# Kernel optimization log

Measured on AMD Instinct MI355X. Metric: run time of the kernel, lower is better.

Reference implementation:

```python
import jax, jax.numpy as jnp
import numpy as np

B_SZ = 4; SEQ = 2048; D_INPUT = 40; D_MODEL = 128; N_LAYERS = 4
D_STATE = 16; EXPAND = 2; D_INNER = D_MODEL * EXPAND
N_HEADS = 4; D_HEAD = D_MODEL // N_HEADS; MAX_LANDMARKS = 100
EPS_RMS = 1.1920929e-07  # torch nn.RMSNorm default eps = finfo(float32).eps
EPS_LN = 1e-5
A_FLOOR = 1e-4


def _rms(x, w):
    return x * jax.lax.rsqrt(jnp.mean(x * x, -1, keepdims=True) + EPS_RMS) * w


def _ln(x, w, b):
    m = jnp.mean(x, -1, keepdims=True)
    v = jnp.mean((x - m) ** 2, -1, keepdims=True)
    return (x - m) * jax.lax.rsqrt(v + EPS_LN) * w + b


def _mamba3_block(xin, Wi, Wx, Wdt, bdt, Alog, Bb, Cb, Bnw, Cnw, rf, Dv, Wo):
    # xin: (B,L,d_model)
    xz = xin @ Wi                       # (B,L,2*d_inner)
    xp, z = jnp.split(xz, 2, axis=-1)
    xp = jax.nn.silu(xp)
    sp = xp @ Wx                        # (B,L,2*d_state+2)
    B_raw = sp[..., :D_STATE]
    C_raw = sp[..., D_STATE:2 * D_STATE]
    dt_in = sp[..., -2:-1]
    lam_in = sp[..., -1:]
    Bm = _rms(B_raw + Bb, Bnw)
    Cm = _rms(C_raw + Cb, Cnw)
    dt = jax.nn.softplus(dt_in @ Wdt + bdt)   # (B,L,d_inner)
    lam = jax.nn.sigmoid(lam_in)              # (B,L,1)
    # data-dependent RoPE on B and C
    freqs = jax.nn.softplus(rf)                                  # (d_state//2,)
    ang = jnp.cumsum(jnp.mean(dt, -1, keepdims=True), axis=1) * freqs  # (B,L,ds/2)
    ca, sa = jnp.cos(ang), jnp.sin(ang)

    def rot(M):
        e, o = M[..., ::2], M[..., 1::2]
        return jnp.stack([e * ca - o * sa, e * sa + o * ca], -1).reshape(M.shape)

    Bm, Cm = rot(Bm), rot(Cm)
    A = jnp.minimum(-jnp.exp(Alog), -A_FLOOR)   # (d_inner,d_state)
    dte = dt[..., None]                          # (B,L,d_inner,1)
    dA = jnp.exp(A * dte)                        # (B,L,d_inner,d_state)
    Bx = Bm[:, :, None, :] * xp[..., None]       # (B,L,d_inner,d_state)
    Bx_prev = jnp.concatenate([jnp.zeros_like(Bx[:, :1]), Bx[:, :-1]], axis=1)
    lame = lam[..., None]                        # (B,L,1,1)
    u = (1.0 - lame) * dte * dA * Bx_prev + lame * dte * Bx
    u = u.at[:, 0].set(dte[:, 0] * Bx[:, 0])     # t==0 case: h = dt*B*x (no lambda)

    def step(h, inp):
        dA_t, u_t, C_t = inp
        h = dA_t * h + u_t
        return h, jnp.sum(h * C_t[:, None, :], -1)

    h0 = jnp.zeros((xin.shape[0], D_INNER, D_STATE), xin.dtype)
    _, ys = jax.lax.scan(step, h0, (jnp.swapaxes(dA, 0, 1), jnp.swapaxes(u, 0, 1), jnp.swapaxes(Cm, 0, 1)))
    y = jnp.swapaxes(ys, 0, 1)                   # (B,L,d_inner)
    y = y + xp * Dv
    y = y * jax.nn.silu(z)
    return y @ Wo


def _landmark_attn(mo, skip, hw, WQ, bQ, WK, bK, WV, bV, WO, bO):
    Bsz, L, Dm = skip.shape
    k = min(MAX_LANDMARKS, L)
    _, idx = jax.lax.top_k(hw, k)
    idx = jnp.sort(idx, axis=1)                            # (B,k)
    kv = jnp.take_along_axis(skip, idx[..., None], axis=1)  # (B,k,Dm)
    q = mo[:, -1:, :]                                       # (B,1,Dm)
    Q = (q @ WQ + bQ).reshape(Bsz, 1, N_HEADS, D_HEAD).transpose(0, 2, 1, 3)
    K = (kv @ WK + bK).reshape(Bsz, k, N_HEADS, D_HEAD).transpose(0, 2, 1, 3)
    V = (kv @ WV + bV).reshape(Bsz, k, N_HEADS, D_HEAD).transpose(0, 2, 1, 3)
    scores = jnp.einsum('bhqd,bhkd->bhqk', Q, K) * (D_HEAD ** -0.5)
    probs = jax.nn.softmax(scores, axis=-1)
    out = jnp.einsum('bhqk,bhkd->bhqd', probs, V).transpose(0, 2, 1, 3).reshape(Bsz, Dm)
    return out @ WO + bO


def setup_inputs() -> dict:
    key = jax.random.key(0)
    ks = iter(jax.random.split(key, 64))

    def nrm(shape, s=0.02):
        return jax.random.normal(next(ks), shape, jnp.float32) * s

    nl, ds, di, dm = N_LAYERS, D_STATE, D_INNER, D_MODEL
    inp = {}
    inp['x'] = jax.random.normal(next(ks), (B_SZ, SEQ, D_INPUT), jnp.float32)
    inp['hawkes_weights'] = jax.random.uniform(next(ks), (B_SZ, SEQ), jnp.float32)
    inp['emb_W'] = nrm((D_INPUT, dm)); inp['emb_b'] = jnp.zeros(dm, jnp.float32)
    inp['skip_W'] = nrm((D_INPUT, dm)); inp['skip_b'] = jnp.zeros(dm, jnp.float32)
    inp['in_proj_W'] = nrm((nl, dm, 2 * di))
    inp['x_proj_W'] = nrm((nl, di, 2 * ds + 2))
    inp['dt_proj_W'] = nrm((nl, 1, di), 1.0)
    inp['dt_proj_b'] = jnp.full((nl, di), -1.0, jnp.float32)
    inp['A_log'] = jnp.broadcast_to(jnp.log(jnp.arange(1, ds + 1, dtype=jnp.float32)), (nl, di, ds)) * jnp.ones((nl, di, ds), jnp.float32)
    inp['B_bias'] = jnp.ones((nl, ds), jnp.float32)
    inp['C_bias'] = jnp.ones((nl, ds), jnp.float32)
    inp['Bn_w'] = jnp.ones((nl, ds), jnp.float32)
    inp['Cn_w'] = jnp.ones((nl, ds), jnp.float32)
    inp['rope_freqs'] = nrm((nl, ds // 2), 0.01)
    inp['D_param'] = jnp.ones((nl, di), jnp.float32)
    inp['out_proj_W'] = nrm((nl, di, dm))
    inp['ln_w'] = jnp.ones((nl, dm), jnp.float32); inp['ln_b'] = jnp.zeros((nl, dm), jnp.float32)
    inp['fn_w'] = jnp.ones(dm, jnp.float32); inp['fn_b'] = jnp.zeros(dm, jnp.float32)
    for nm in ('Q', 'K', 'V', 'O'):
        inp['W' + nm] = nrm((dm, dm)); inp['b' + nm] = jnp.zeros(dm, jnp.float32)
    return inp


def reference(x, hawkes_weights, emb_W, emb_b, skip_W, skip_b, in_proj_W, x_proj_W,
              dt_proj_W, dt_proj_b, A_log, B_bias, C_bias, Bn_w, Cn_w, rope_freqs,
              D_param, out_proj_W, ln_w, ln_b, fn_w, fn_b, WQ, bQ, WK, bK, WV, bV, WO, bO):
    w = hawkes_weights[..., None]
    h = (x @ emb_W + emb_b) * w          # Hawkes-damped embedding for Mamba path
    skip = (x @ skip_W + skip_b) * w     # Hawkes skip for attention KV
    for i in range(N_LAYERS):
        h = h + _mamba3_block(_ln(h, ln_w[i], ln_b[i]), in_proj_W[i], x_proj_W[i],
                              dt_proj_W[i], dt_proj_b[i], A_log[i], B_bias[i], C_bias[i],
                              Bn_w[i], Cn_w[i], rope_freqs[i], D_param[i], out_proj_W[i])
    mo = _ln(h, fn_w, fn_b)
    return _landmark_attn(mo, skip, hawkes_weights, WQ, bQ, WK, bK, WV, bV, WO, bO)
```

## Files before the change

### kernel.cpp

```cpp
#include <hip/hip_runtime.h>
#include <math.h>

#define BSZ   4
#define SEQL  2048
#define DIN   40
#define DM    128
#define DI    256
#define DS    16
#define NL    4
#define NHEAD 4
#define DHEAD 32
#define KLM   100
#define NC    128
#define TC    16
#define NROWS 8

__device__ __forceinline__ float sigmoidf_(float x){ return 1.0f/(1.0f + expf(-x)); }
__device__ __forceinline__ float siluf_(float x){ return x/(1.0f + expf(-x)); }
__device__ __forceinline__ float softplusf_(float x){ return fmaxf(x,0.0f) + log1pf(expf(-fabsf(x))); }

__device__ __forceinline__ float block_sum256(float v, float* red){
  #pragma unroll
  for (int o=32;o>0;o>>=1) v += __shfl_down(v,o,64);
  __syncthreads();
  if ((threadIdx.x & 63)==0) red[threadIdx.x>>6] = v;
  __syncthreads();
  return red[0]+red[1]+red[2]+red[3];
}
__device__ __forceinline__ int block_isum256(int v, int* red){
  #pragma unroll
  for (int o=32;o>0;o>>=1) v += __shfl_down(v,o,64);
  __syncthreads();
  if ((threadIdx.x & 63)==0) red[threadIdx.x>>6] = v;
  __syncthreads();
  return red[0]+red[1]+red[2]+red[3];
}
__device__ __forceinline__ void load16(const float* p, float* r){
  const float4* q = (const float4*)p;
  float4 a=q[0], b=q[1], c=q[2], d=q[3];
  r[0]=a.x;r[1]=a.y;r[2]=a.z;r[3]=a.w; r[4]=b.x;r[5]=b.y;r[6]=b.z;r[7]=b.w;
  r[8]=c.x;r[9]=c.y;r[10]=c.z;r[11]=c.w; r[12]=d.x;r[13]=d.y;r[14]=d.z;r[15]=d.w;
}
__device__ __forceinline__ void store16(float* p, const float* r){
  float4* q = (float4*)p;
  q[0]=make_float4(r[0],r[1],r[2],r[3]);  q[1]=make_float4(r[4],r[5],r[6],r[7]);
  q[2]=make_float4(r[8],r[9],r[10],r[11]);q[3]=make_float4(r[12],r[13],r[14],r[15]);
}

__global__ __launch_bounds__(128) void embed_kernel(
    const float* __restrict__ x, const float* __restrict__ hw,
    const float* __restrict__ eW, const float* __restrict__ eb,
    const float* __restrict__ sW, const float* __restrict__ sb,
    float* __restrict__ hb, float* __restrict__ sk)
{
  __shared__ float xr[DIN];
  const size_t R = blockIdx.x;
  const int t = threadIdx.x;
  if (t < DIN) xr[t] = x[R*DIN + t];
  __syncthreads();
  float a = eb[t], s = sb[t];
  #pragma unroll 8
  for (int k=0;k<DIN;k++){
    const float xv = xr[k];
    a = fmaf(xv, eW[(size_t)k*DM + t], a);
    s = fmaf(xv, sW[(size_t)k*DM + t], s);
  }
  const float w = hw[R];
  hb[R*DM + t] = a*w;
  sk[R*DM + t] = s*w;
}

__global__ __launch_bounds__(256) void pre_kernel(
    const float* __restrict__ hb,
    const float* __restrict__ Wi, const float* __restrict__ Wx,
    const float* __restrict__ Wdt, const float* __restrict__ bdt,
    const float* __restrict__ Bb, const float* __restrict__ Cb,
    const float* __restrict__ Bnw, const float* __restrict__ Cnw,
    const float* __restrict__ lnw, const float* __restrict__ lnb,
    float* __restrict__ xpb, float* __restrict__ zsb, float* __restrict__ dtb,
    float* __restrict__ Bmb, float* __restrict__ Cmb,
    float* __restrict__ lamb, float* __restrict__ mdtb)
{
  __shared__ float xin[NROWS][DM];
  __shared__ float xps[NROWS][DI+2];
  __shared__ float spl[NROWS][40];
  __shared__ float red_f[4];

  const int t = threadIdx.x;
  const size_t R0 = (size_t)blockIdx.x * NROWS;

  {
    const int r = t >> 5, j = t & 31;
    const float4 v = ((const float4*)(hb + (R0 + r)*DM))[j];
    float s = v.x+v.y+v.z+v.w;
    #pragma unroll
    for (int o=16;o>0;o>>=1) s += __shfl_xor(s,o,32);
    const float m = s*(1.0f/DM);
    const float dx=v.x-m, dy=v.y-m, dz=v.z-m, dw=v.w-m;
    float ss = dx*dx+dy*dy+dz*dz+dw*dw;
    #pragma unroll
    for (int o=16;o>0;o>>=1) ss += __shfl_xor(ss,o,32);
    const float inv = 1.0f/sqrtf(ss*(1.0f/DM) + 1e-5f);
    const int c = j*4;
    xin[r][c+0] = dx*inv*lnw[c+0] + lnb[c+0];
    xin[r][c+1] = dy*inv*lnw[c+1] + lnb[c+1];
    xin[r][c+2] = dz*inv*lnw[c+2] + lnb[c+2];
    xin[r][c+3] = dw*inv*lnw[c+3] + lnb[c+3];
  }
  __syncthreads();

  {
    float a0[NROWS], a1[NROWS];
    #pragma unroll
    for (int r=0;r<NROWS;r++){ a0[r]=0.0f; a1[r]=0.0f; }
    for (int k=0;k<DM;k++){
      const float w0 = Wi[(size_t)k*(2*DI) + t];
      const float w1 = Wi[(size_t)k*(2*DI) + DI + t];
      #pragma unroll
      for (int r=0;r<NROWS;r++){
        const float xv = xin[r][k];
        a0[r] = fmaf(xv, w0, a0[r]);
        a1[r] = fmaf(xv, w1, a1[r]);
      }
    }
    #pragma unroll
    for (int r=0;r<NROWS;r++){
      const float xpv = siluf_(a0[r]);
      const float zv  = siluf_(a1[r]);
      xps[r][t] = xpv;
      xpb[(R0+r)*DI + t] = xpv;
      zsb[(R0+r)*DI + t] = zv;
    }
  }
  __syncthreads();

  for (int task=t; task<NROWS*34; task+=256){
    const int r = task/34, o2 = task - r*34;
    float a = 0.0f;
    #pragma unroll 8
    for (int k=0;k<DI;k++) a = fmaf(xps[r][k], Wx[(size_t)k*34 + o2], a);
    spl[r][o2] = a;
  }
  __syncthreads();

  {
    const int half = t >> 7;
    const int r = (t >> 4) & 7, s = t & 15;
    const float* bias = half ? Cb : Bb;
    const float* wn   = half ? Cnw : Bnw;
    const float v = spl[r][half*DS + s] + bias[s];
    float ss = v*v;
    #pragma unroll
    for (int o=8;o>0;o>>=1) ss += __shfl_xor(ss,o,16);
    const float inv = 1.0f/sqrtf(ss*(1.0f/DS) + 1.1920929e-07f);
    (half ? Cmb : Bmb)[(R0+r)*DS + s] = v*inv*wn[s];
  }

  const float wdt = Wdt[t], bdtv = bdt[t];
  for (int r=0;r<NROWS;r++){
    const float dval = softplusf_(fmaf(spl[r][32], wdt, bdtv));
    dtb[(R0+r)*DI + t] = dval;
    const float s = block_sum256(dval, red_f);
    if (t == 0){
      mdtb[R0+r] = s*(1.0f/DI);
      lamb[R0+r] = sigmoidf_(spl[r][33]);
    }
  }
}

__global__ __launch_bounds__(256) void cumsum_kernel(const float* __restrict__ mdt, double* __restrict__ angs){
  __shared__ double part[256];
  const int b = blockIdx.x, t = threadIdx.x;
  const float* p = mdt + (size_t)b*SEQL;
  double vals[8], loc = 0.0;
  #pragma unroll
  for (int q=0;q<8;q++){ vals[q] = (double)p[t*8+q]; loc += vals[q]; }
  part[t] = loc;
  __syncthreads();
  for (int o=1;o<256;o<<=1){
    const double add = (t>=o) ? part[t-o] : 0.0;
    __syncthreads();
    part[t] += add;
    __syncthreads();
  }
  double run = part[t] - loc;
  double* ap = angs + (size_t)b*SEQL + (size_t)t*8;
  #pragma unroll
  for (int q=0;q<8;q++){ run += vals[q]; ap[q] = run; }
}

__global__ __launch_bounds__(256) void rot_kernel(
    const double* __restrict__ angs, const float* __restrict__ rf,
    float* __restrict__ Bmb, float* __restrict__ Cmb)
{
  const int id = blockIdx.x*256 + threadIdx.x;
  const int f = id & 7;
  const size_t R = (size_t)(id >> 3);
  const double xfr = (double)rf[f];
  const double fq = fmax(xfr, 0.0) + log1p(exp(-fabs(xfr)));
  const double a = angs[R]*fq;
  const float ca = (float)cos(a), sa = (float)sin(a);
  float e = Bmb[R*DS + 2*f], o = Bmb[R*DS + 2*f + 1];
  Bmb[R*DS + 2*f]     = e*ca - o*sa;
  Bmb[R*DS + 2*f + 1] = e*sa + o*ca;
  e = Cmb[R*DS + 2*f]; o = Cmb[R*DS + 2*f + 1];
  Cmb[R*DS + 2*f]     = e*ca - o*sa;
  Cmb[R*DS + 2*f + 1] = e*sa + o*ca;
}

__global__ __launch_bounds__(256) void scan1_kernel(
    const float* __restrict__ xp, const float* __restrict__ dtb,
    const float* __restrict__ Bmb, const float* __restrict__ lamb,
    const float* __restrict__ Alog, float* __restrict__ hend, float* __restrict__ Pp)
{
  const int id = blockIdx.x*256 + threadIdx.x;
  const int d = id & (DI-1);
  const int c = (id >> 8) & (NC-1);
  const int b = id >> 15;
  float A[DS];
  #pragma unroll
  for (int s=0;s<DS;s++) A[s] = fminf(-expf(Alog[d*DS+s]), -1e-4f);
  const size_t bL = (size_t)b*SEQL;
  const int t0 = c*TC;
  float h[DS], P[DS], Bprev[DS];
  #pragma unroll
  for (int s=0;s<DS;s++){ h[s]=0.0f; P[s]=1.0f; Bprev[s]=0.0f; }
  float xpm1 = 0.0f;
  int tstart = t0;
  if (t0 > 0){
    load16(Bmb + (bL + t0 - 1)*DS, Bprev);
    xpm1 = xp[(bL + t0 - 1)*DI + d];
  } else {
    const size_t rowE = bL*DI + d;
    const float dtv = dtb[rowE];
    const float xpv = xp[rowE];
    float Bcur[DS]; load16(Bmb + bL*DS, Bcur);
    #pragma unroll
    for (int s=0;s<DS;s++){
      const float a = __expf(A[s]*dtv);
      h[s] = dtv*(Bcur[s]*xpv);
      P[s] *= a;
      Bprev[s] = Bcur[s];
    }
    xpm1 = xpv;
    tstart = 1;
  }
  for (int t=tstart; t<t0+TC; ++t){
    const size_t rowE = (bL + t)*DI + d;
    const float dtv = dtb[rowE];
    const float xpv = xp[rowE];
    const float lamv = lamb[bL + t];
    float Bcur[DS]; load16(Bmb + (bL + t)*DS, Bcur);
    const float dl = dtv*lamv;
    const float dml = dtv - dl;
    const float bxp_s = xpm1, bx_s = xpv;
    #pragma unroll
    for (int s=0;s<DS;s++){
      const float a = __expf(A[s]*dtv);
      const float u = fmaf(dml*a, Bprev[s]*bxp_s, dl*(Bcur[s]*bx_s));
      h[s] = fmaf(a, h[s], u);
      P[s] *= a;
      Bprev[s] = Bcur[s];
    }
    xpm1 = xpv;
  }
  store16(hend + (size_t)id*DS, h);
  store16(Pp   + (size_t)id*DS, P);
}

__global__ __launch_bounds__(256) void scan2_kernel(float* __restrict__ hend, const float* __restrict__ Pp){
  const int id = blockIdx.x*256 + threadIdx.x;
  const int s = id & 15, d = (id >> 4) & (DI-1), b = id >> 12;
  float H = 0.0f;
  #pragma unroll 4
  for (int c=0;c<NC;c++){
    const size_t ix = (((size_t)(b*NC + c))*DI + d)*DS + s;
    const float he = hend[ix], p = Pp[ix];
    hend[ix] = H;
    H = fmaf(p, H, he);
  }
}

__global__ __launch_bounds__(256) void scan3_kernel(
    const float* __restrict__ xp, float* __restrict__ dty,
    const float* __restrict__ Bmb, const float* __restrict__ Cmb,
    const float* __restrict__ lamb, const float* __restrict__ zsb,
    const float* __restrict__ Alog, const float* __restrict__ Dv,
    const float* __restrict__ Hin)
{
  const int id = blockIdx.x*256 + threadIdx.x;
  const int d = id & (DI-1);
  const int c = (id >> 8) & (NC-1);
  const int b = id >> 15;
  float A[DS];
  #pragma unroll
  for (int s=0;s<DS;s++) A[s] = fminf(-expf(Alog[d*DS+s]), -1e-4f);
  const float dvp = Dv[d];
  const size_t bL = (size_t)b*SEQL;
  const int t0 = c*TC;
  float h[DS], Bprev[DS];
  load16(Hin + (size_t)id*DS, h);
  #pragma unroll
  for (int s=0;s<DS;s++) Bprev[s]=0.0f;
  float xpm1 = 0.0f;
  int tstart = t0;
  if (t0 > 0){
    load16(Bmb + (bL + t0 - 1)*DS, Bprev);
    xpm1 = xp[(bL + t0 - 1)*DI + d];
  } else {
    const size_t rowE = bL*DI + d;
    const float dtv = dty[rowE];
    const float xpv = xp[rowE];
    float Bcur[DS]; load16(Bmb + bL*DS, Bcur);
    float Ccur[DS]; load16(Cmb + bL*DS, Ccur);
    float y = 0.0f;
    #pragma unroll
    for (int s=0;s<DS;s++){
      h[s] = dtv*(Bcur[s]*xpv);
      y = fmaf(h[s], Ccur[s], y);
      Bprev[s] = Bcur[s];
    }
    dty[rowE] = (y + xpv*dvp)*zsb[rowE];
    xpm1 = xpv;
    tstart = 1;
  }
  for (int t=tstart; t<t0+TC; ++t){
    const size_t rowE = (bL + t)*DI + d;
    const float dtv = dty[rowE];
    const float xpv = xp[rowE];
    const float lamv = lamb[bL + t];
    float Bcur[DS]; load16(Bmb + (bL + t)*DS, Bcur);
    float Ccur[DS]; load16(Cmb + (bL + t)*DS, Ccur);
    const float dl = dtv*lamv;
    const float dml = dtv - dl;
    float y = 0.0f;
    #pragma unroll
    for (int s=0;s<DS;s++){
      const float a = __expf(A[s]*dtv);
      const float u = fmaf(dml*a, Bprev[s]*xpm1, dl*(Bcur[s]*xpv));
      h[s] = fmaf(a, h[s], u);
      y = fmaf(h[s], Ccur[s], y);
      Bprev[s] = Bcur[s];
    }
    dty[rowE] = (y + xpv*dvp)*zsb[rowE];
    xpm1 = xpv;
  }
}

__global__ __launch_bounds__(256) void post_kernel(
    const float* __restrict__ yb, const float* __restrict__ Wo,
    float* __restrict__ hb)
{
  __shared__ float yl[NROWS][DI+2];
  const int t = threadIdx.x;
  const size_t R0 = (size_t)blockIdx.x * NROWS;
  #pragma unroll
  for (int r=0;r<NROWS;r++) yl[r][t] = yb[(R0+r)*DI + t];
  __syncthreads();
  const int c = t & (DM-1), g = t >> 7;
  float acc[4] = {0.0f,0.0f,0.0f,0.0f};
  for (int k=0;k<DI;k++){
    const float wv = Wo[(size_t)k*DM + c];
    #pragma unroll
    for (int rr=0;rr<4;rr++) acc[rr] = fmaf(yl[g + rr*2][k], wv, acc[rr]);
  }
  #pragma unroll
  for (int rr=0;rr<4;rr++) hb[(R0 + g + rr*2)*DM + c] += acc[rr];
}

__global__ __launch_bounds__(256) void attn_kernel(
    const float* __restrict__ hb, const float* __restrict__ sk,
    const float* __restrict__ hw,
    const float* __restrict__ fnw, const float* __restrict__ fnb,
    const float* __restrict__ WQ, const float* __restrict__ bQ,
    const float* __restrict__ WK, const float* __restrict__ bK,
    const float* __restrict__ WV, const float* __restrict__ bV,
    const float* __restrict__ WO, const float* __restrict__ bO,
    float* __restrict__ outp)
{
  __shared__ float kv[KLM][DM+1];
  __shared__ float mo[DM];
  __shared__ float Qs[DM];
  __shared__ float qk[NHEAD][DM];
  __shared__ float bterm[NHEAD];
  __shared__ float sc[NHEAD][KLM];
  __shared__ float pbar[NHEAD][DM];
  __shared__ float attno[DM];
  __shared__ int idxl[KLM];
  __shared__ int red_i[4];
  __shared__ float red_f[4];

  const int b = blockIdx.x;
  const int t = threadIdx.x;
  const int lane = t & 63, w = t >> 6;

  const float* hwp = hw + (size_t)b*SEQL;
  unsigned vb[8];
  #pragma unroll
  for (int q=0;q<8;q++) vb[q] = __float_as_uint(hwp[q*256 + t]);

  unsigned kth = 0u;
  for (int bit=31; bit>=0; --bit){
    const unsigned cand = kth | (1u << bit);
    int c0 = 0;
    #pragma unroll
    for (int q=0;q<8;q++) c0 += (vb[q] >= cand) ? 1 : 0;
    if (block_isum256(c0, red_i) >= KLM) kth = cand;
  }
  int cg0 = 0;
  #pragma unroll
  for (int q=0;q<8;q++) cg0 += (vb[q] > kth) ? 1 : 0;
  const int cnt_gt = block_isum256(cg0, red_i);
  const int need_eq = KLM - cnt_gt;

  int eq_base = 0, sel_base = 0;
  for (int r=0;r<8;r++){
    const bool eq = (vb[r] == kth);
    const bool gt = (vb[r] >  kth);
    const unsigned long long mEq = __ballot(eq);
    __syncthreads();
    if (lane==0) red_i[w] = __popcll(mEq);
    __syncthreads();
    int eqBefore = eq_base + __popcll(mEq & ((1ull<<lane)-1ull));
    for (int j=0;j<w;j++) eqBefore += red_i[j];
    const int eqTot = red_i[0]+red_i[1]+red_i[2]+red_i[3];
    const bool sel = gt || (eq && eqBefore < need_eq);
    const unsigned long long mSel = __ballot(sel);
    __syncthreads();
    if (lane==0) red_i[w] = __popcll(mSel);
    __syncthreads();
    int pos = sel_base + __popcll(mSel & ((1ull<<lane)-1ull));
    for (int j=0;j<w;j++) pos += red_i[j];
    const int selTot = red_i[0]+red_i[1]+red_i[2]+red_i[3];
    if (sel && pos < KLM) idxl[pos] = r*256 + t;
    eq_base += eqTot; sel_base += selTot;
  }
  __syncthreads();

  {
    const float* hr = hb + ((size_t)b*SEQL + (SEQL-1))*DM;
    const float hv = (t < DM) ? hr[t] : 0.0f;
    const float ssum = block_sum256(hv, red_f);
    const float mean = ssum*(1.0f/DM);
    const float dv = (t < DM) ? (hv - mean) : 0.0f;
    const float vsum = block_sum256(dv*dv, red_f);
    const float inv = 1.0f/sqrtf(vsum*(1.0f/DM) + 1e-5f);
    if (t < DM) mo[t] = dv*inv*fnw[t] + fnb[t];
  }
  __syncthreads();

  for (int e=t; e<KLM*DM; e+=256){
    const int j = e >> 7, cc = e & (DM-1);
    kv[j][cc] = sk[((size_t)b*SEQL + idxl[j])*DM + cc];
  }
  __syncthreads();

  if (t < DM){
    float a = bQ[t];
    #pragma unroll 4
    for (int k=0;k<DM;k++) a = fmaf(mo[k], WQ[(size_t)k*DM + t], a);
    Qs[t] = a;
  }
  __syncthreads();
  for (int e=t; e<NHEAD*DM; e+=256){
    const int hh = e >> 7, m = e & (DM-1);
    const int c0 = hh*DHEAD;
    float a = 0.0f;
    #pragma unroll
    for (int cc=0; cc<DHEAD; cc++) a = fmaf(WK[(size_t)m*DM + c0 + cc], Qs[c0+cc], a);
    qk[hh][m] = a;
  }
  if (t < NHEAD){
    float a = 0.0f;
    for (int cc=0; cc<DHEAD; cc++) a += bK[t*DHEAD+cc]*Qs[t*DHEAD+cc];
    bterm[t] = a;
  }
  __syncthreads();
  for (int e=t; e<NHEAD*KLM; e+=256){
    const int hh = e/KLM, j = e - hh*KLM;
    float a = bterm[hh];
    #pragma unroll 4
    for (int m=0;m<DM;m++) a = fmaf(kv[j][m], qk[hh][m], a);
    sc[hh][j] = a*0.17677669529663687f;
  }
  __syncthreads();
  {
    const int hh = w;
    const float v0 = (lane < KLM) ? sc[hh][lane] : -3.0e38f;
    const float v1 = (lane+64 < KLM) ? sc[hh][lane+64] : -3.0e38f;
    float mx = fmaxf(v0, v1);
    #pragma unroll
    for (int o2=32;o2>0;o2>>=1) mx = fmaxf(mx, __shfl_xor(mx,o2,64));
    const float e0 = (lane < KLM) ? expf(v0-mx) : 0.0f;
    const float e1 = (lane+64 < KLM) ? expf(v1-mx) : 0.0f;
    float sm = e0+e1;
    #pragma unroll
    for (int o2=32;o2>0;o2>>=1) sm += __shfl_xor(sm,o2,64);
    const float inv2 = 1.0f/sm;
    if (lane < KLM) sc[hh][lane] = e0*inv2;
    if (lane+64 < KLM) sc[hh][lane+64] = e1*inv2;
  }
  __syncthreads();
  for (int e=t; e<NHEAD*DM; e+=256){
    const int hh = e >> 7, m = e & (DM-1);
    float a = 0.0f;
    #pragma unroll 4
    for (int j=0;j<KLM;j++) a = fmaf(sc[hh][j], kv[j][m], a);
    pbar[hh][m] = a;
  }
  __syncthreads();
  if (t < DM){
    const int hh = t >> 5;
    float a = bV[t];
    #pragma unroll 4
    for (int m=0;m<DM;m++) a = fmaf(pbar[hh][m], WV[(size_t)m*DM + t], a);
    attno[t] = a;
  }
  __syncthreads();
  if (t < DM){
    float a = bO[t];
    #pragma unroll 4
    for (int c2=0;c2<DM;c2++) a = fmaf(attno[c2], WO[(size_t)c2*DM + t], a);
    outp[(size_t)b*DM + t] = a;
  }
}

extern "C" void kernel_launch(void* const* d_in, const int* in_sizes, int n_in,
                              void* d_out, int out_size, void* d_ws, size_t ws_size,
                              hipStream_t stream)
{
  (void)in_sizes; (void)n_in; (void)out_size; (void)ws_size;
  const float* x    = (const float*)d_in[0];
  const float* hw   = (const float*)d_in[1];
  const float* embW = (const float*)d_in[2];
  const float* embB = (const float*)d_in[3];
  const float* skW  = (const float*)d_in[4];
  const float* skB  = (const float*)d_in[5];
  const float* inW  = (const float*)d_in[6];
  const float* xpW  = (const float*)d_in[7];
  const float* dtW  = (const float*)d_in[8];
  const float* dtB  = (const float*)d_in[9];
  const float* Alog = (const float*)d_in[10];
  const float* Bb   = (const float*)d_in[11];
  const float* Cb   = (const float*)d_in[12];
  const float* Bnw  = (const float*)d_in[13];
  const float* Cnw  = (const float*)d_in[14];
  const float* rf   = (const float*)d_in[15];
  const float* Dpar = (const float*)d_in[16];
  const float* outW = (const float*)d_in[17];
  const float* lnW  = (const float*)d_in[18];
  const float* lnB  = (const float*)d_in[19];
  const float* fnW  = (const float*)d_in[20];
  const float* fnB  = (const float*)d_in[21];
  const float* WQ = (const float*)d_in[22]; const float* bQ = (const float*)d_in[23];
  const float* WK = (const float*)d_in[24]; const float* bK = (const float*)d_in[25];
  const float* WV = (const float*)d_in[26]; const float* bV = (const float*)d_in[27];
  const float* WO = (const float*)d_in[28]; const float* bO = (const float*)d_in[29];

  float* ws = (float*)d_ws;
  size_t off = 0;
  float* hb   = ws + off; off += (size_t)BSZ*SEQL*DM;
  float* sk   = ws + off; off += (size_t)BSZ*SEQL*DM;
  float* xpb  = ws + off; off += (size_t)BSZ*SEQL*DI;
  float* zsb  = ws + off; off += (size_t)BSZ*SEQL*DI;
  float* dtb  = ws + off; off += (size_t)BSZ*SEQL*DI;
  float* Bmb  = ws + off; off += (size_t)BSZ*SEQL*DS;
  float* Cmb  = ws + off; off += (size_t)BSZ*SEQL*DS;
  float* lamb = ws + off; off += (size_t)BSZ*SEQL;
  float* mdtb = ws + off; off += (size_t)BSZ*SEQL;
  float* hend = ws + off; off += (size_t)BSZ*NC*DI*DS;
  float* Ppb  = ws + off; off += (size_t)BSZ*NC*DI*DS;
  double* angs = (double*)(ws + off);

  embed_kernel<<<BSZ*SEQL, DM, 0, stream>>>(x, hw, embW, embB, skW, skB, hb, sk);

  for (int i=0;i<NL;i++){
    pre_kernel<<<BSZ*SEQL/NROWS, 256, 0, stream>>>(hb,
        inW + (size_t)i*DM*2*DI, xpW + (size_t)i*DI*34,
        dtW + (size_t)i*DI, dtB + (size_t)i*DI,
        Bb + i*DS, Cb + i*DS, Bnw + i*DS, Cnw + i*DS,
        lnW + i*DM, lnB + i*DM,
        xpb, zsb, dtb, Bmb, Cmb, lamb, mdtb);
    cumsum_kernel<<<BSZ, 256, 0, stream>>>(mdtb, angs);
    rot_kernel<<<BSZ*SEQL*8/256, 256, 0, stream>>>(angs, rf + i*8, Bmb, Cmb);
    scan1_kernel<<<BSZ*NC*DI/256, 256, 0, stream>>>(xpb, dtb, Bmb, lamb,
        Alog + (size_t)i*DI*DS, hend, Ppb);
    scan2_kernel<<<BSZ*DI*DS/256, 256, 0, stream>>>(hend, Ppb);
    scan3_kernel<<<BSZ*NC*DI/256, 256, 0, stream>>>(xpb, dtb, Bmb, Cmb, lamb, zsb,
        Alog + (size_t)i*DI*DS, Dpar + (size_t)i*DI, hend);
    post_kernel<<<BSZ*SEQL/NROWS, 256, 0, stream>>>(dtb, outW + (size_t)i*DI*DM, hb);
  }

  attn_kernel<<<BSZ, 256, 0, stream>>>(hb, sk, hw, fnW, fnB,
      WQ, bQ, WK, bK, WV, bV, WO, bO, (float*)d_out);
}
```

Baseline: 579.3 us.

## Fuse cumsum with rotation and scan3 with output projection, restructure several kernels

Merges the cumsum and RoPE-rotation kernels into one wave-shuffle scan kernel that uses fast sincos after range reduction. It also fuses the final scan pass with the output projection, so y stays in shared memory instead of a global round trip. Separately, embed processes 16 rows per block, pre_kernel transposes Wx into shared memory and vectorises its matmuls, the scans stage B/C/lambda in shared memory, and the attention top-k selection uses ballots with fewer barriers. Swapping double-precision cos/sin for float __sincosf after reduction may slightly change accuracy of the RoPE angles.

```diff
diff --git a/kernel.cpp b/kernel.cpp
--- a/kernel.cpp
+++ b/kernel.cpp
@@ -14,20 +14,13 @@
 #define NC    128
 #define TC    16
 #define NROWS 8
+#define EROWS 16
 
 __device__ __forceinline__ float sigmoidf_(float x){ return 1.0f/(1.0f + expf(-x)); }
 __device__ __forceinline__ float siluf_(float x){ return x/(1.0f + expf(-x)); }
 __device__ __forceinline__ float softplusf_(float x){ return fmaxf(x,0.0f) + log1pf(expf(-fabsf(x))); }
 
 __device__ __forceinline__ float block_sum256(float v, float* red){
-  #pragma unroll
-  for (int o=32;o>0;o>>=1) v += __shfl_down(v,o,64);
-  __syncthreads();
-  if ((threadIdx.x & 63)==0) red[threadIdx.x>>6] = v;
-  __syncthreads();
-  return red[0]+red[1]+red[2]+red[3];
-}
-__device__ __forceinline__ int block_isum256(int v, int* red){
   #pragma unroll
   for (int o=32;o>0;o>>=1) v += __shfl_down(v,o,64);
   __syncthreads();
@@ -47,27 +40,39 @@
   q[2]=make_float4(r[8],r[9],r[10],r[11]);q[3]=make_float4(r[12],r[13],r[14],r[15]);
 }
 
-__global__ __launch_bounds__(128) void embed_kernel(
+__global__ __launch_bounds__(256) void embed_kernel(
     const float* __restrict__ x, const float* __restrict__ hw,
     const float* __restrict__ eW, const float* __restrict__ eb,
     const float* __restrict__ sW, const float* __restrict__ sb,
     float* __restrict__ hb, float* __restrict__ sk)
 {
-  __shared__ float xr[DIN];
-  const size_t R = blockIdx.x;
+  __shared__ float xr[EROWS][DIN];
   const int t = threadIdx.x;
-  if (t < DIN) xr[t] = x[R*DIN + t];
-  __syncthreads();
-  float a = eb[t], s = sb[t];
-  #pragma unroll 8
+  const size_t R0 = (size_t)blockIdx.x * EROWS;
+  for (int e=t; e<EROWS*DIN; e+=256) ((float*)xr)[e] = x[R0*DIN + e];
+  __syncthreads();
+  const int c = t & (DM-1), g = t >> 7;
+  float ae[8], as[8];
+  #pragma unroll
+  for (int j=0;j<8;j++){ ae[j]=0.0f; as[j]=0.0f; }
   for (int k=0;k<DIN;k++){
-    const float xv = xr[k];
-    a = fmaf(xv, eW[(size_t)k*DM + t], a);
-    s = fmaf(xv, sW[(size_t)k*DM + t], s);
-  }
-  const float w = hw[R];
-  hb[R*DM + t] = a*w;
-  sk[R*DM + t] = s*w;
+    const float we  = eW[(size_t)k*DM + c];
+    const float ws_ = sW[(size_t)k*DM + c];
+    #pragma unroll
+    for (int j=0;j<8;j++){
+      const float xv = xr[g*8+j][k];
+      ae[j] = fmaf(xv, we, ae[j]);
+      as[j] = fmaf(xv, ws_, as[j]);
+    }
+  }
+  const float ebv = eb[c], sbv = sb[c];
+  #pragma unroll
+  for (int j=0;j<8;j++){
+    const size_t R = R0 + g*8 + j;
+    const float w = hw[R];
+    hb[R*DM + c] = (ae[j]+ebv)*w;
+    sk[R*DM + c] = (as[j]+sbv)*w;
+  }
 }
 
 __global__ __launch_bounds__(256) void pre_kernel(
@@ -81,10 +86,10 @@
     float* __restrict__ Bmb, float* __restrict__ Cmb,
     float* __restrict__ lamb, float* __restrict__ mdtb)
 {
-  __shared__ float xin[NROWS][DM];
-  __shared__ float xps[NROWS][DI+2];
+  __shared__ float xin[NROWS][DM+4];
+  __shared__ float xps[NROWS][DI+4];
+  __shared__ float WxT[34][DI+4];
   __shared__ float spl[NROWS][40];
-  __shared__ float red_f[4];
 
   const int t = threadIdx.x;
   const size_t R0 = (size_t)blockIdx.x * NROWS;
@@ -107,105 +112,152 @@
     xin[r][c+2] = dz*inv*lnw[c+2] + lnb[c+2];
     xin[r][c+3] = dw*inv*lnw[c+3] + lnb[c+3];
   }
-  __syncthreads();
-
-  {
-    float a0[NROWS], a1[NROWS];
-    #pragma unroll
-    for (int r=0;r<NROWS;r++){ a0[r]=0.0f; a1[r]=0.0f; }
-    for (int k=0;k<DM;k++){
-      const float w0 = Wi[(size_t)k*(2*DI) + t];
-      const float w1 = Wi[(size_t)k*(2*DI) + DI + t];
+  for (int e=t; e<DI*34; e+=256){
+    const int d = e/34, o = e - d*34;
+    WxT[o][d] = Wx[e];
+  }
+  __syncthreads();
+
+  {
+    float2 a[NROWS];
+    #pragma unroll
+    for (int r=0;r<NROWS;r++){ a[r].x=0.0f; a[r].y=0.0f; }
+    for (int k=0;k<DM;k+=4){
+      const float2 w0 = *(const float2*)&Wi[(size_t)(k+0)*(2*DI) + 2*t];
+      const float2 w1 = *(const float2*)&Wi[(size_t)(k+1)*(2*DI) + 2*t];
+      const float2 w2 = *(const float2*)&Wi[(size_t)(k+2)*(2*DI) + 2*t];
+      const float2 w3 = *(const float2*)&Wi[(size_t)(k+3)*(2*DI) + 2*t];
       #pragma unroll
       for (int r=0;r<NROWS;r++){
-        const float xv = xin[r][k];
-        a0[r] = fmaf(xv, w0, a0[r]);
-        a1[r] = fmaf(xv, w1, a1[r]);
+        const float4 xv = *(const float4*)&xin[r][k];
+        a[r].x = fmaf(xv.x,w0.x,a[r].x); a[r].y = fmaf(xv.x,w0.y,a[r].y);
+        a[r].x = fmaf(xv.y,w1.x,a[r].x); a[r].y = fmaf(xv.y,w1.y,a[r].y);
+        a[r].x = fmaf(xv.z,w2.x,a[r].x); a[r].y = fmaf(xv.z,w2.y,a[r].y);
+        a[r].x = fmaf(xv.w,w3.x,a[r].x); a[r].y = fmaf(xv.w,w3.y,a[r].y);
       }
     }
-    #pragma unroll
-    for (int r=0;r<NROWS;r++){
-      const float xpv = siluf_(a0[r]);
-      const float zv  = siluf_(a1[r]);
-      xps[r][t] = xpv;
-      xpb[(R0+r)*DI + t] = xpv;
-      zsb[(R0+r)*DI + t] = zv;
-    }
-  }
-  __syncthreads();
-
-  for (int task=t; task<NROWS*34; task+=256){
-    const int r = task/34, o2 = task - r*34;
-    float a = 0.0f;
-    #pragma unroll 8
-    for (int k=0;k<DI;k++) a = fmaf(xps[r][k], Wx[(size_t)k*34 + o2], a);
-    spl[r][o2] = a;
+    if (t < 128){
+      #pragma unroll
+      for (int r=0;r<NROWS;r++){
+        float2 s; s.x = siluf_(a[r].x); s.y = siluf_(a[r].y);
+        xps[r][2*t] = s.x; xps[r][2*t+1] = s.y;
+        *(float2*)&xpb[(R0+r)*DI + 2*t] = s;
+      }
+    } else {
+      const int c = 2*t - DI;
+      #pragma unroll
+      for (int r=0;r<NROWS;r++){
+        float2 s; s.x = siluf_(a[r].x); s.y = siluf_(a[r].y);
+        *(float2*)&zsb[(R0+r)*DI + c] = s;
+      }
+    }
+  }
+  __syncthreads();
+
+  for (int task=t; task<272; task+=256){
+    const int o = task >> 3, r = task & 7;
+    float acc = 0.0f;
+    for (int k=0;k<DI;k+=4){
+      const float4 xv = *(const float4*)&xps[r][k];
+      const float4 wv = *(const float4*)&WxT[o][k];
+      acc = fmaf(xv.x,wv.x,acc); acc = fmaf(xv.y,wv.y,acc);
+      acc = fmaf(xv.z,wv.z,acc); acc = fmaf(xv.w,wv.w,acc);
+    }
+    spl[r][o] = acc;
   }
   __syncthreads();
 
   {
     const int half = t >> 7;
-    const int r = (t >> 4) & 7, s = t & 15;
+    const int r2 = (t >> 4) & 7, s2 = t & 15;
     const float* bias = half ? Cb : Bb;
     const float* wn   = half ? Cnw : Bnw;
-    const float v = spl[r][half*DS + s] + bias[s];
+    const float v = spl[r2][half*DS + s2] + bias[s2];
     float ss = v*v;
     #pragma unroll
     for (int o=8;o>0;o>>=1) ss += __shfl_xor(ss,o,16);
     const float inv = 1.0f/sqrtf(ss*(1.0f/DS) + 1.1920929e-07f);
-    (half ? Cmb : Bmb)[(R0+r)*DS + s] = v*inv*wn[s];
-  }
-
-  const float wdt = Wdt[t], bdtv = bdt[t];
-  for (int r=0;r<NROWS;r++){
-    const float dval = softplusf_(fmaf(spl[r][32], wdt, bdtv));
-    dtb[(R0+r)*DI + t] = dval;
-    const float s = block_sum256(dval, red_f);
-    if (t == 0){
-      mdtb[R0+r] = s*(1.0f/DI);
-      lamb[R0+r] = sigmoidf_(spl[r][33]);
-    }
-  }
-}
-
-__global__ __launch_bounds__(256) void cumsum_kernel(const float* __restrict__ mdt, double* __restrict__ angs){
-  __shared__ double part[256];
-  const int b = blockIdx.x, t = threadIdx.x;
-  const float* p = mdt + (size_t)b*SEQL;
-  double vals[8], loc = 0.0;
-  #pragma unroll
-  for (int q=0;q<8;q++){ vals[q] = (double)p[t*8+q]; loc += vals[q]; }
-  part[t] = loc;
-  __syncthreads();
-  for (int o=1;o<256;o<<=1){
-    const double add = (t>=o) ? part[t-o] : 0.0;
-    __syncthreads();
-    part[t] += add;
-    __syncthreads();
-  }
-  double run = part[t] - loc;
-  double* ap = angs + (size_t)b*SEQL + (size_t)t*8;
-  #pragma unroll
-  for (int q=0;q<8;q++){ run += vals[q]; ap[q] = run; }
-}
-
-__global__ __launch_bounds__(256) void rot_kernel(
-    const double* __restrict__ angs, const float* __restrict__ rf,
+    (half ? Cmb : Bmb)[(R0+r2)*DS + s2] = v*inv*wn[s2];
+  }
+
+  float (*sred)[DI+4] = WxT;
+  {
+    const float wdt = Wdt[t], bdtv = bdt[t];
+    #pragma unroll
+    for (int r=0;r<NROWS;r++){
+      const float dval = softplusf_(fmaf(spl[r][32], wdt, bdtv));
+      dtb[(R0+r)*DI + t] = dval;
+      sred[r][t] = dval;
+    }
+    if (t < NROWS) lamb[R0+t] = sigmoidf_(spl[t][33]);
+  }
+  __syncthreads();
+
+  {
+    const int lane = t & 63, w = t >> 6;
+    #pragma unroll
+    for (int rr=0;rr<2;rr++){
+      const int row = 2*w + rr;
+      float s = sred[row][lane] + sred[row][lane+64] + sred[row][lane+128] + sred[row][lane+192];
+      #pragma unroll
+      for (int o=32;o>0;o>>=1) s += __shfl_xor(s,o,64);
+      if (lane==0) mdtb[R0+row] = s*(1.0f/DI);
+    }
+  }
+}
+
+__global__ __launch_bounds__(1024) void cumrot_kernel(
+    const float* __restrict__ mdt, const float* __restrict__ rf,
     float* __restrict__ Bmb, float* __restrict__ Cmb)
 {
-  const int id = blockIdx.x*256 + threadIdx.x;
-  const int f = id & 7;
-  const size_t R = (size_t)(id >> 3);
-  const double xfr = (double)rf[f];
-  const double fq = fmax(xfr, 0.0) + log1p(exp(-fabs(xfr)));
-  const double a = angs[R]*fq;
-  const float ca = (float)cos(a), sa = (float)sin(a);
-  float e = Bmb[R*DS + 2*f], o = Bmb[R*DS + 2*f + 1];
-  Bmb[R*DS + 2*f]     = e*ca - o*sa;
-  Bmb[R*DS + 2*f + 1] = e*sa + o*ca;
-  e = Cmb[R*DS + 2*f]; o = Cmb[R*DS + 2*f + 1];
-  Cmb[R*DS + 2*f]     = e*ca - o*sa;
-  Cmb[R*DS + 2*f + 1] = e*sa + o*ca;
+  __shared__ double wsum[16];
+  __shared__ double fqs[8];
+  const int b = blockIdx.x, t = threadIdx.x;
+  const int lane = t & 63, w = t >> 6;
+  if (t < 8){
+    const double xfr = (double)rf[t];
+    fqs[t] = fmax(xfr, 0.0) + log1p(exp(-fabs(xfr)));
+  }
+  const float* p = mdt + (size_t)b*SEQL;
+  const double v0 = (double)p[2*t], v1 = (double)p[2*t+1];
+  double acc = v0 + v1;
+  #pragma unroll
+  for (int o=1;o<64;o<<=1){
+    const double nb = __shfl_up(acc, o, 64);
+    if (lane >= o) acc += nb;
+  }
+  if (lane==63) wsum[w] = acc;
+  __syncthreads();
+  double woff = 0.0;
+  for (int j=0;j<w;j++) woff += wsum[j];
+  const double inc1 = woff + acc;
+  const double inc0 = inc1 - v1;
+  const double TWO_PI = 6.283185307179586;
+  const double INV2PI = 0.15915494309189535;
+  #pragma unroll
+  for (int rr=0;rr<2;rr++){
+    const double ab = rr ? inc1 : inc0;
+    const size_t row = (size_t)b*SEQL + 2*t + rr;
+    float ca[8], sa[8];
+    #pragma unroll
+    for (int f=0; f<8; f++){
+      const double ang = ab * fqs[f];
+      const double red = ang - floor(ang*INV2PI)*TWO_PI;
+      __sincosf((float)red, &sa[f], &ca[f]);
+    }
+    float B[16], C[16];
+    load16(Bmb + row*DS, B); load16(Cmb + row*DS, C);
+    #pragma unroll
+    for (int f=0; f<8; f++){
+      const float be=B[2*f], bo=B[2*f+1];
+      B[2*f]   = be*ca[f] - bo*sa[f];
+      B[2*f+1] = be*sa[f] + bo*ca[f];
+      const float ce=C[2*f], co=C[2*f+1];
+      C[2*f]   = ce*ca[f] - co*sa[f];
+      C[2*f+1] = ce*sa[f] + co*ca[f];
+    }
+    store16(Bmb + row*DS, B); store16(Cmb + row*DS, C);
+  }
 }
 
 __global__ __launch_bounds__(256) void scan1_kernel(
@@ -213,54 +265,67 @@
     const float* __restrict__ Bmb, const float* __restrict__ lamb,
     const float* __restrict__ Alog, float* __restrict__ hend, float* __restrict__ Pp)
 {
-  const int id = blockIdx.x*256 + threadIdx.x;
-  const int d = id & (DI-1);
-  const int c = (id >> 8) & (NC-1);
-  const int b = id >> 15;
-  float A[DS];
-  #pragma unroll
-  for (int s=0;s<DS;s++) A[s] = fminf(-expf(Alog[d*DS+s]), -1e-4f);
+  __shared__ float Bst[TC+1][DS];
+  __shared__ float lst[TC];
+  const int t = threadIdx.x;
+  const int d = t;
+  const int c = blockIdx.x & (NC-1);
+  const int b = blockIdx.x >> 7;
   const size_t bL = (size_t)b*SEQL;
   const int t0 = c*TC;
+  const int id = blockIdx.x*256 + t;
+
+  for (int e=t; e<(TC+1)*DS; e+=256){
+    const int j = e >> 4, s = e & 15;
+    const int trow = t0 - 1 + j;
+    Bst[j][s] = (trow >= 0) ? Bmb[(bL + trow)*DS + s] : 0.0f;
+  }
+  if (t < TC) lst[t] = lamb[bL + t0 + t];
+  __syncthreads();
+
+  float A[DS];
+  #pragma unroll
+  for (int s=0;s<DS;s++) A[s] = fminf(-expf(Alog[d*DS+s]), -1e-4f);
   float h[DS], P[DS], Bprev[DS];
   #pragma unroll
-  for (int s=0;s<DS;s++){ h[s]=0.0f; P[s]=1.0f; Bprev[s]=0.0f; }
-  float xpm1 = 0.0f;
-  int tstart = t0;
+  for (int s=0;s<DS;s++){ h[s]=0.0f; P[s]=1.0f; }
+  float xpm1;
+  int tstart;
   if (t0 > 0){
-    load16(Bmb + (bL + t0 - 1)*DS, Bprev);
+    #pragma unroll
+    for (int s=0;s<DS;s++) Bprev[s] = Bst[0][s];
     xpm1 = xp[(bL + t0 - 1)*DI + d];
+    tstart = t0;
   } else {
     const size_t rowE = bL*DI + d;
     const float dtv = dtb[rowE];
     const float xpv = xp[rowE];
-    float Bcur[DS]; load16(Bmb + bL*DS, Bcur);
     #pragma unroll
     for (int s=0;s<DS;s++){
       const float a = __expf(A[s]*dtv);
-      h[s] = dtv*(Bcur[s]*xpv);
+      h[s] = dtv*(Bst[1][s]*xpv);
       P[s] *= a;
-      Bprev[s] = Bcur[s];
+      Bprev[s] = Bst[1][s];
     }
     xpm1 = xpv;
     tstart = 1;
   }
-  for (int t=tstart; t<t0+TC; ++t){
-    const size_t rowE = (bL + t)*DI + d;
+  for (int tt=tstart; tt<t0+TC; ++tt){
+    const size_t rowE = (bL + tt)*DI + d;
     const float dtv = dtb[rowE];
     const float xpv = xp[rowE];
-    const float lamv = lamb[bL + t];
-    float Bcur[DS]; load16(Bmb + (bL + t)*DS, Bcur);
+    const float lamv = lst[tt - t0];
+    const int j = tt - t0 + 1;
     const float dl = dtv*lamv;
     const float dml = dtv - dl;
-    const float bxp_s = xpm1, bx_s = xpv;
     #pragma unroll
     for (int s=0;s<DS;s++){
       const float a = __expf(A[s]*dtv);
-      const float u = fmaf(dml*a, Bprev[s]*bxp_s, dl*(Bcur[s]*bx_s));
+      const float Bc = Bst[j][s];
+      const float u = fmaf(dml*a, Bprev[s]*xpm1, dl*(Bc*xpv));
       h[s] = fmaf(a, h[s], u);
       P[s] *= a;
-      Bprev[s] = Bcur[s];
+      Bprev[s] = Bc;
     }
     xpm1 = xpv;
   }
@@ -281,91 +346,114 @@
   }
 }
 
-__global__ __launch_bounds__(256) void scan3_kernel(
-    const float* __restrict__ xp, float* __restrict__ dty,
+__global__ __launch_bounds__(256) void scan3post_kernel(
+    const float* __restrict__ xp, const float* __restrict__ dtb,
     const float* __restrict__ Bmb, const float* __restrict__ Cmb,
     const float* __restrict__ lamb, const float* __restrict__ zsb,
     const float* __restrict__ Alog, const float* __restrict__ Dv,
-    const float* __restrict__ Hin)
+    const float* __restrict__ Hin, const float* __restrict__ Wo,
+    float* __restrict__ hb)
 {
-  const int id = blockIdx.x*256 + threadIdx.x;
-  const int d = id & (DI-1);
-  const int c = (id >> 8) & (NC-1);
-  const int b = id >> 15;
+  __shared__ float Bst[TC+1][DS];
+  __shared__ float Cst[TC][DS];
+  __shared__ float lst[TC];
+  __shared__ float ys[TC][DI+4];
+  const int t = threadIdx.x;
+  const int d = t;
+  const int c = blockIdx.x & (NC-1);
+  const int b = blockIdx.x >> 7;
+  const size_t bL = (size_t)b*SEQL;
+  const int t0 = c*TC;
+  const int id = blockIdx.x*256 + t;
+
+  for (int e=t; e<(TC+1)*DS; e+=256){
+    const int j = e >> 4, s = e & 15;
+    const int trow = t0 - 1 + j;
+    Bst[j][s] = (trow >= 0) ? Bmb[(bL + trow)*DS + s] : 0.0f;
+    if (j < TC) Cst[j][s] = Cmb[(bL + t0 + j)*DS + s];
+  }
+  if (t < TC) lst[t] = lamb[bL + t0 + t];
+  __syncthreads();
+
   float A[DS];
   #pragma unroll
   for (int s=0;s<DS;s++) A[s] = fminf(-expf(Alog[d*DS+s]), -1e-4f);
   const float dvp = Dv[d];
-  const size_t bL = (size_t)b*SEQL;
-  const int t0 = c*TC;
   float h[DS], Bprev[DS];
   load16(Hin + (size_t)id*DS, h);
-  #pragma unroll
-  for (int s=0;s<DS;s++) Bprev[s]=0.0f;
-  float xpm1 = 0.0f;
-  int tstart = t0;
+  float xpm1;
+  int tstart;
   if (t0 > 0){
-    load16(Bmb + (bL + t0 - 1)*DS, Bprev);
+    #pragma unroll
+    for (int s=0;s<DS;s++) Bprev[s] = Bst[0][s];
     xpm1 = xp[(bL + t0 - 1)*DI + d];
+    tstart = t0;
   } else {
     const size_t rowE = bL*DI + d;
-    const float dtv = dty[rowE];
+    const float dtv = dtb[rowE];
     const float xpv = xp[rowE];
-    float Bcur[DS]; load16(Bmb + bL*DS, Bcur);
-    float Ccur[DS]; load16(Cmb + bL*DS, Ccur);
     float y = 0.0f;
     #pragma unroll
     for (int s=0;s<DS;s++){
-      h[s] = dtv*(Bcur[s]*xpv);
-      y = fmaf(h[s], Ccur[s], y);
-      Bprev[s] = Bcur[s];
-    }
-    dty[rowE] = (y + xpv*dvp)*zsb[rowE];
+      h[s] = dtv*(Bst[1][s]*xpv);
+      y = fmaf(h[s], Cst[0][s], y);
+      Bprev[s] = Bst[1][s];
+    }
+    ys[0][d] = (y + xpv*dvp)*zsb[rowE];
     xpm1 = xpv;
     tstart = 1;
   }
-  for (int t=tstart; t<t0+TC; ++t){
-    const size_t rowE = (bL + t)*DI + d;
-    const float dtv = dty[rowE];
+  for (int tt=tstart; tt<t0+TC; ++tt){
+    const size_t rowE = (bL + tt)*DI + d;
+    const float dtv = dtb[rowE];
     const float xpv = xp[rowE];
-    const float lamv = lamb[bL + t];
-    float Bcur[DS]; load16(Bmb + (bL + t)*DS, Bcur);
-    float Ccur[DS]; load16(Cmb + (bL + t)*DS, Ccur);
+    const float lamv = lst[tt - t0];
+    const int j = tt - t0;
     const float dl = dtv*lamv;
     const float dml = dtv - dl;
     float y = 0.0f;
     #pragma unroll
     for (int s=0;s<DS;s++){
       const float a = __expf(A[s]*dtv);
-      const float u = fmaf(dml*a, Bprev[s]*xpm1, dl*(Bcur[s]*xpv));
+      const float Bc = Bst[j+1][s];
+      const float u = fmaf(dml*a, Bprev[s]*xpm1, dl*(Bc*xpv));
       h[s] = fmaf(a, h[s], u);
-      y = fmaf(h[s], Ccur[s], y);
-      Bprev[s] = Bcur[s];
-    }
-    dty[rowE] = (y + xpv*dvp)*zsb[rowE];
+      y = fmaf(h[s], Cst[j][s], y);
+      Bprev[s] = Bc;
+    }
+    ys[j][d] = (y + xpv*dvp)*zsb[rowE];
     xpm1 = xpv;
   }
-}
-
-__global__ __launch_bounds__(256) void post_kernel(
-    const float* __restrict__ yb, const float* __restrict__ Wo,
-    float* __restrict__ hb)
-{
-  __shared__ float yl[NROWS][DI+2];
-  const int t = threadIdx.x;
-  const size_t R0 = (size_t)blockIdx.x * NROWS;
-  #pragma unroll
-  for (int r=0;r<NROWS;r++) yl[r][t] = yb[(R0+r)*DI + t];
-  __syncthreads();
-  const int c = t & (DM-1), g = t >> 7;
-  float acc[4] = {0.0f,0.0f,0.0f,0.0f};
-  for (int k=0;k<DI;k++){
-    const float wv = Wo[(size_t)k*DM + c];
-    #pragma unroll
-    for (int rr=0;rr<4;rr++) acc[rr] = fmaf(yl[g + rr*2][k], wv, acc[rr]);
-  }
-  #pragma unroll
-  for (int rr=0;rr<4;rr++) hb[(R0 + g + rr*2)*DM + c] += acc[rr];
+  __syncthreads();
+
+  {
+    const int r  = t >> 4;
+    const int cg = t & 15;
+    const int c0 = cg*8;
+    float acc[8];
+    #pragma unroll
+    for (int j=0;j<8;j++) acc[j]=0.0f;
+    for (int k=0;k<DI;k+=4){
+      const float4 yv = *(const float4*)&ys[r][k];
+      const float yy[4] = {yv.x, yv.y, yv.z, yv.w};
+      #pragma unroll
+      for (int j=0;j<4;j++){
+        const float4 wa = *(const float4*)&Wo[(size_t)(k+j)*DM + c0];
+        const float4 wb = *(const float4*)&Wo[(size_t)(k+j)*DM + c0 + 4];
+        acc[0]=fmaf(yy[j],wa.x,acc[0]); acc[1]=fmaf(yy[j],wa.y,acc[1]);
+        acc[2]=fmaf(yy[j],wa.z,acc[2]); acc[3]=fmaf(yy[j],wa.w,acc[3]);
+        acc[4]=fmaf(yy[j],wb.x,acc[4]); acc[5]=fmaf(yy[j],wb.y,acc[5]);
+        acc[6]=fmaf(yy[j],wb.z,acc[6]); acc[7]=fmaf(yy[j],wb.w,acc[7]);
+      }
+    }
+    const size_t row = bL + t0 + r;
+    float4 h0 = *(const float4*)&hb[row*DM + c0];
+    float4 h1 = *(const float4*)&hb[row*DM + c0 + 4];
+    h0.x+=acc[0]; h0.y+=acc[1]; h0.z+=acc[2]; h0.w+=acc[3];
+    h1.x+=acc[4]; h1.y+=acc[5]; h1.z+=acc[6]; h1.w+=acc[7];
+    *(float4*)&hb[row*DM + c0]     = h0;
+    *(float4*)&hb[row*DM + c0 + 4] = h1;
+  }
 }
 
 __global__ __launch_bounds__(256) void attn_kernel(
@@ -378,7 +466,7 @@
     const float* __restrict__ WO, const float* __restrict__ bO,
     float* __restrict__ outp)
 {
-  __shared__ float kv[KLM][DM+1];
+  __shared__ float kv[KLM][DM+4];
   __shared__ float mo[DM];
   __shared__ float Qs[DM];
   __shared__ float qk[NHEAD][DM];
@@ -387,7 +475,8 @@
   __shared__ float pbar[NHEAD][DM];
   __shared__ float attno[DM];
   __shared__ int idxl[KLM];
-  __shared__ int red_i[4];
+  __shared__ int redcnt[2][4];
+  __shared__ int eqc[8][4], gtc[8][4];
   __shared__ float red_f[4];
 
   const int b = blockIdx.x;
@@ -404,36 +493,48 @@
     const unsigned cand = kth | (1u << bit);
     int c0 = 0;
     #pragma unroll
-    for (int q=0;q<8;q++) c0 += (vb[q] >= cand) ? 1 : 0;
-    if (block_isum256(c0, red_i) >= KLM) kth = cand;
-  }
-  int cg0 = 0;
-  #pragma unroll
-  for (int q=0;q<8;q++) cg0 += (vb[q] > kth) ? 1 : 0;
-  const int cnt_gt = block_isum256(cg0, red_i);
-  const int need_eq = KLM - cnt_gt;
-
-  int eq_base = 0, sel_base = 0;
-  for (int r=0;r<8;r++){
-    const bool eq = (vb[r] == kth);
-    const bool gt = (vb[r] >  kth);
-    const unsigned long long mEq = __ballot(eq);
+    for (int q=0;q<8;q++) c0 += __popcll(__ballot(vb[q] >= cand));
+    const int par = bit & 1;
+    if (lane == 0) redcnt[par][w] = c0;
     __syncthreads();
-    if (lane==0) red_i[w] = __popcll(mEq);
-    __syncthreads();
-    int eqBefore = eq_base + __popcll(mEq & ((1ull<<lane)-1ull));
-    for (int j=0;j<w;j++) eqBefore += red_i[j];
-    const int eqTot = red_i[0]+red_i[1]+red_i[2]+red_i[3];
-    const bool sel = gt || (eq && eqBefore < need_eq);
-    const unsigned long long mSel = __ballot(sel);
-    __syncthreads();
-    if (lane==0) red_i[w] = __popcll(mSel);
-    __syncthreads();
-    int pos = sel_base + __popcll(mSel & ((1ull<<lane)-1ull));
-    for (int j=0;j<w;j++) pos += red_i[j];
-    const int selTot = red_i[0]+red_i[1]+red_i[2]+red_i[3];
-    if (sel && pos < KLM) idxl[pos] = r*256 + t;
-    eq_base += eqTot; sel_base += selTot;
+    const int tot = redcnt[par][0]+redcnt[par][1]+redcnt[par][2]+redcnt[par][3];
+    if (tot >= KLM) kth = cand;
+  }
+
+  unsigned long long beq[8], bgt[8];
+  #pragma unroll
+  for (int q=0;q<8;q++){
+    beq[q] = __ballot(vb[q] == kth);
+    bgt[q] = __ballot(vb[q] >  kth);
+  }
+  if (lane == 0){
+    #pragma unroll
+    for (int q=0;q<8;q++){ eqc[q][w] = __popcll(beq[q]); gtc[q][w] = __popcll(bgt[q]); }
+  }
+  __syncthreads();
+  {
+    int gtTot = 0;
+    #pragma unroll
+    for (int q=0;q<8;q++) gtTot += gtc[q][0]+gtc[q][1]+gtc[q][2]+gtc[q][3];
+    const int need_eq = KLM - gtTot;
+    const unsigned long long lmask = (lane==0) ? 0ull : ((~0ull) >> (64-lane));
+    int eqPfx = 0, gtPfx = 0;
+    #pragma unroll
+    for (int q=0;q<8;q++){
+      int eqWP = 0, gtWP = 0;
+      for (int w2=0; w2<w; ++w2){ eqWP += eqc[q][w2]; gtWP += gtc[q][w2]; }
+      const int eqBefore = eqPfx + eqWP + __popcll(beq[q] & lmask);
+      const int gtBefore = gtPfx + gtWP + __popcll(bgt[q] & lmask);
+      if (vb[q] > kth){
+        const int pos = gtBefore + min(eqBefore, need_eq);
+        if (pos < KLM) idxl[pos] = q*256 + t;
+      } else if (vb[q] == kth && eqBefore < need_eq){
+        const int pos = gtBefore + eqBefore;
+        if (pos < KLM) idxl[pos] = q*256 + t;
+      }
+      eqPfx += eqc[q][0]+eqc[q][1]+eqc[q][2]+eqc[q][3];
+      gtPfx += gtc[q][0]+gtc[q][1]+gtc[q][2]+gtc[q][3];
+    }
   }
   __syncthreads();
 
@@ -479,8 +580,12 @@
   for (int e=t; e<NHEAD*KLM; e+=256){
     const int hh = e/KLM, j = e - hh*KLM;
     float a = bterm[hh];
-    #pragma unroll 4
-    for (int m=0;m<DM;m++) a = fmaf(kv[j][m], qk[hh][m], a);
+    for (int m=0;m<DM;m+=4){
+      const float4 kvv = *(const float4*)&kv[j][m];
+      const float4 qv  = *(const float4*)&qk[hh][m];
+      a = fmaf(kvv.x,qv.x,a); a = fmaf(kvv.y,qv.y,a);
+      a = fmaf(kvv.z,qv.z,a); a = fmaf(kvv.w,qv.w,a);
+    }
     sc[hh][j] = a*0.17677669529663687f;
   }
   __syncthreads();
@@ -512,8 +617,13 @@
   if (t < DM){
     const int hh = t >> 5;
     float a = bV[t];
-    #pragma unroll 4
-    for (int m=0;m<DM;m++) a = fmaf(pbar[hh][m], WV[(size_t)m*DM + t], a);
+    for (int m=0;m<DM;m+=4){
+      const float4 pv = *(const float4*)&pbar[hh][m];
+      a = fmaf(pv.x, WV[(size_t)(m+0)*DM + t], a);
+      a = fmaf(pv.y, WV[(size_t)(m+1)*DM + t], a);
+      a = fmaf(pv.z, WV[(size_t)(m+2)*DM + t], a);
+      a = fmaf(pv.w, WV[(size_t)(m+3)*DM + t], a);
+    }
     attno[t] = a;
   }
   __syncthreads();
@@ -570,9 +680,8 @@
   float* mdtb = ws + off; off += (size_t)BSZ*SEQL;
   float* hend = ws + off; off += (size_t)BSZ*NC*DI*DS;
   float* Ppb  = ws + off; off += (size_t)BSZ*NC*DI*DS;
-  double* angs = (double*)(ws + off);
-
-  embed_kernel<<<BSZ*SEQL, DM, 0, stream>>>(x, hw, embW, embB, skW, skB, hb, sk);
+
+  embed_kernel<<<BSZ*SEQL/EROWS, 256, 0, stream>>>(x, hw, embW, embB, skW, skB, hb, sk);
 
   for (int i=0;i<NL;i++){
     pre_kernel<<<BSZ*SEQL/NROWS, 256, 0, stream>>>(hb,
@@ -581,14 +690,13 @@
         Bb + i*DS, Cb + i*DS, Bnw + i*DS, Cnw + i*DS,
         lnW + i*DM, lnB + i*DM,
         xpb, zsb, dtb, Bmb, Cmb, lamb, mdtb);
-    cumsum_kernel<<<BSZ, 256, 0, stream>>>(mdtb, angs);
-    rot_kernel<<<BSZ*SEQL*8/256, 256, 0, stream>>>(angs, rf + i*8, Bmb, Cmb);
-    scan1_kernel<<<BSZ*NC*DI/256, 256, 0, stream>>>(xpb, dtb, Bmb, lamb,
+    cumrot_kernel<<<BSZ, 1024, 0, stream>>>(mdtb, rf + i*8, Bmb, Cmb);
+    scan1_kernel<<<BSZ*NC, 256, 0, stream>>>(xpb, dtb, Bmb, lamb,
         Alog + (size_t)i*DI*DS, hend, Ppb);
     scan2_kernel<<<BSZ*DI*DS/256, 256, 0, stream>>>(hend, Ppb);
-    scan3_kernel<<<BSZ*NC*DI/256, 256, 0, stream>>>(xpb, dtb, Bmb, Cmb, lamb, zsb,
-        Alog + (size_t)i*DI*DS, Dpar + (size_t)i*DI, hend);
-    post_kernel<<<BSZ*SEQL/NROWS, 256, 0, stream>>>(dtb, outW + (size_t)i*DI*DM, hb);
+    scan3post_kernel<<<BSZ*NC, 256, 0, stream>>>(xpb, dtb, Bmb, Cmb, lamb, zsb,
+        Alog + (size_t)i*DI*DS, Dpar + (size_t)i*DI, hend,
+        outW + (size_t)i*DI*DM, hb);
   }
 
   attn_kernel<<<BSZ, 256, 0, stream>>>(hb, sk, hw, fnW, fnB,
```

Measured after the change: 648.3 us. 1.12x slower.
